# Kernel tuning notes

Measured on AMD Instinct MI355X. Metric: run time of the kernel, lower is better.

## Reference

```python
import jax, jax.numpy as jnp
import numpy as np

V, D, NL, S, B = 32000, 1024, 2, 2048, 1
EXPAND, N, K = 2, 16, 4
DI = EXPAND * D
EPS = 1e-5


def setup_inputs() -> dict:
    key = jax.random.key(0)
    ks = jax.random.split(key, 10)
    std = 0.02
    inp = {
        "input_ids": jax.random.randint(ks[0], (B, S), 0, V),
        "embedding": jax.random.normal(ks[1], (V, D), jnp.float32) * std,
        "in_proj_w": jax.random.normal(ks[2], (NL, 2 * DI, D), jnp.float32) * std,
        "conv_w": jax.random.normal(ks[3], (NL, DI, 1, K), jnp.float32) * std,
        "conv_b": jnp.zeros((NL, DI), jnp.float32),
        "x_proj_w": jax.random.normal(ks[4], (NL, 2 * N, DI), jnp.float32) * std,
        "dt_proj_w": jax.random.normal(ks[5], (NL, DI, DI), jnp.float32) * std,
        "dt_proj_b": jnp.zeros((NL, DI), jnp.float32),
        "A_log": jnp.broadcast_to(jnp.log(jnp.arange(1, N + 1, dtype=jnp.float32)), (NL, DI, N)).copy(),
        "D_param": jnp.ones((NL, DI), jnp.float32),
        "out_proj_w": jax.random.normal(ks[6], (NL, D, DI), jnp.float32) * std,
        "norm_w": jnp.ones((NL, D), jnp.float32),
        "norm_f_w": jnp.ones((D,), jnp.float32),
        "lm_head_w": jax.random.normal(ks[7], (V, D), jnp.float32) * std,
    }
    return inp


def rmsnorm(x, w):
    rms = jnp.sqrt(jnp.mean(x * x, axis=-1, keepdims=True) + EPS)
    return x / rms * w


def silu(x):
    return x * jax.nn.sigmoid(x)


def ssm_layer(x, in_w, cw, cb, xp_w, dt_w, dt_b, A_log, Dp):
    b, s, _ = x.shape
    xz = jnp.einsum("bsd,ed->bse", x, in_w)  # (B,S,2*DI)
    xi, z = jnp.split(xz, 2, axis=-1)
    # depthwise causal conv1d
    xc = jnp.swapaxes(xi, 1, 2)  # (B,DI,S)
    xc = jax.lax.conv_general_dilated(
        xc, cw, window_strides=(1,), padding=[(K - 1, 0)],
        dimension_numbers=("NCH", "OIH", "NCH"), feature_group_count=DI,
    ) + cb[None, :, None]
    xi = silu(jnp.swapaxes(xc, 1, 2))  # (B,S,DI)
    bc = jnp.einsum("bsd,ed->bse", xi, xp_w)  # (B,S,2N)
    Bc, Cc = jnp.split(bc, 2, axis=-1)
    dt = jax.nn.softplus(jnp.einsum("bsd,ed->bse", xi, dt_w) + dt_b)
    A = -jnp.exp(A_log)  # (DI,N)
    dA = jnp.exp(dt[..., None] * A)                      # (B,S,DI,N)
    dBu = dt[..., None] * Bc[:, :, None, :] * xi[..., None]  # (B,S,DI,N)

    def step(h, t):
        dA_t, dBu_t, C_t, u_t = t
        h = dA_t * h + dBu_t                     # (B,DI,N)
        y = jnp.sum(h * C_t[:, None, :], axis=-1) + Dp * u_t  # (B,DI)
        return h, y

    xs = (jnp.swapaxes(dA, 0, 1), jnp.swapaxes(dBu, 0, 1),
          jnp.swapaxes(Cc, 0, 1), jnp.swapaxes(xi, 0, 1))
    h0 = jnp.zeros((b, DI, N), x.dtype)
    _, ys = jax.lax.scan(step, h0, xs)
    y = jnp.swapaxes(ys, 0, 1)  # (B,S,DI)
    y = y * silu(z)
    return y


def reference(input_ids, embedding, in_proj_w, conv_w, conv_b, x_proj_w,
              dt_proj_w, dt_proj_b, A_log, D_param, out_proj_w, norm_w,
              norm_f_w, lm_head_w):
    x = embedding[input_ids]  # (B,S,D)
    for l in range(NL):
        h = rmsnorm(x, norm_w[l])
        y = ssm_layer(h, in_proj_w[l], conv_w[l], conv_b[l], x_proj_w[l],
                      dt_proj_w[l], dt_proj_b[l], A_log[l], D_param[l])
        x = x + jnp.einsum("bse,de->bsd", y, out_proj_w[l])
    x = rmsnorm(x, norm_f_w)
    logits = jnp.einsum("bsd,vd->bsv", x, lm_head_w)
    return logits
```

## Files before the change

kernel.cpp:

```cpp
#include <hip/hip_runtime.h>
#include <hip/hip_bf16.h>
#include <stdint.h>
#include <stddef.h>

#define Vv   32000
#define Dd   1024
#define NLay 2
#define Ss   2048
#define Nn   16
#define Kc   4
#define DIc  2048
#define EPSf 1e-5f
#define LCH  32
#define NCHc (Ss / LCH)
#define CATR 2176

typedef __attribute__((ext_vector_type(8))) short bf16x8;
typedef __attribute__((ext_vector_type(4))) float f32x4;

__device__ __forceinline__ short f2bf(float f) {
  union { float f; unsigned u; } a; a.f = f;
  return (short)((a.u + 0x7FFFu + ((a.u >> 16) & 1u)) >> 16);
}
__device__ __forceinline__ float bf2f(short s) {
  union { unsigned u; float f; } a; a.u = ((unsigned)(unsigned short)s) << 16;
  return a.f;
}

struct CvtSeg { const float* s; short* d; unsigned n4; };
struct CvtBatch { CvtSeg seg[7]; unsigned tot4; };
__global__ __launch_bounds__(256) void cvt_all_k(CvtBatch b) {
  for (unsigned idx = blockIdx.x * 256 + threadIdx.x; idx < b.tot4;
       idx += gridDim.x * 256) {
    unsigned r = idx;
    int sg = 0;
    while (sg < 6 && r >= b.seg[sg].n4) { r -= b.seg[sg].n4; ++sg; }
    float4 v = ((const float4*)b.seg[sg].s)[r];
    short4 o;
    o.x = f2bf(v.x); o.y = f2bf(v.y); o.z = f2bf(v.z); o.w = f2bf(v.w);
    ((short4*)b.seg[sg].d)[r] = o;
  }
}

__global__ __launch_bounds__(256) void embed_k(const int* __restrict__ ids,
                                               const float* __restrict__ emb,
                                               float* __restrict__ x) {
  int s = blockIdx.x;
  int id = ids[s];
  const float4* src = (const float4*)(emb + (size_t)id * Dd);
  float4* dst = (float4*)(x + (size_t)s * Dd);
  dst[threadIdx.x] = src[threadIdx.x];
}

__global__ __launch_bounds__(256) void rmsnorm_k(const float* __restrict__ x,
                                                 const float* __restrict__ w,
                                                 short* __restrict__ o) {
  int s = blockIdx.x, t = threadIdx.x;
  float4 v = ((const float4*)(x + (size_t)s * Dd))[t];
  float ss = v.x * v.x + v.y * v.y + v.z * v.z + v.w * v.w;
#pragma unroll
  for (int off = 32; off; off >>= 1) ss += __shfl_down(ss, off);
  __shared__ float red[4];
  if ((t & 63) == 0) red[t >> 6] = ss;
  __syncthreads();
  ss = red[0] + red[1] + red[2] + red[3];
  float rinv = rsqrtf(ss * (1.0f / Dd) + EPSf);
  float4 wv = ((const float4*)w)[t];
  short4 ov;
  ov.x = f2bf(v.x * rinv * wv.x);
  ov.y = f2bf(v.y * rinv * wv.y);
  ov.z = f2bf(v.z * rinv * wv.z);
  ov.w = f2bf(v.w * rinv * wv.w);
  ((short4*)(o + (size_t)s * Dd))[t] = ov;
}

template <int BM, int BN, int WM, int WN, bool RESID, bool CAT>
__global__ __launch_bounds__(256) void gemm_bt(const short* __restrict__ A,
                                               const short* __restrict__ B,
                                               float* C, const float* __restrict__ resb,
                                               float* C2, int M, int N, int K, int nMt) {
  constexpr int BK = 32;
  constexpr int FM = BM / (WM * 16);
  constexpr int FN = BN / (WN * 16);
  constexpr int A_SLOTS = BM * (BK / 8);
  constexpr int B_SLOTS = BN * (BK / 8);
  __shared__ short sA[BM * BK];
  __shared__ short sB[BN * BK];
  const int t = threadIdx.x;
  const int lane = t & 63;
  const int w = t >> 6;
  const int wm = w / WN, wn = w % WN;
  const int nwg = gridDim.x;
  const int chunk = nwg >> 3;
  const int wg = (blockIdx.x & 7) * chunk + (blockIdx.x >> 3);
  const int mi = wg % nMt;
  const int ni = wg / nMt;
  const int rowBase = mi * BM;
  const int colBase = ni * BN;
  const int l4 = lane >> 4;
  const int lr = lane & 15;
  const int mrd = ((lr & 3) ^ ((lr >> 2) & 1));

  f32x4 acc[FM][FN];
#pragma unroll
  for (int i = 0; i < FM; i++)
#pragma unroll
    for (int j = 0; j < FN; j++) acc[i][j] = f32x4{0.f, 0.f, 0.f, 0.f};

  for (int k0 = 0; k0 < K; k0 += BK) {
    __syncthreads();
#pragma unroll
    for (int i = 0; i < (A_SLOTS + 255) / 256; i++) {
      int q = i * 256 + t;
      if (A_SLOTS % 256 == 0 || q < A_SLOTS) {
        int row = q >> 2, ps = q & 3;
        int ls = ps ^ ((row & 3) ^ ((row >> 2) & 1));
        const short* src = A + (size_t)(rowBase + row) * K + (k0 + ls * 8);
        __builtin_amdgcn_global_load_lds(
            (__attribute__((address_space(1))) unsigned int*)src,
            (__attribute__((address_space(3))) unsigned int*)(sA + q * 8), 16, 0, 0);
      }
    }
#pragma unroll
    for (int i = 0; i < (B_SLOTS + 255) / 256; i++) {
      int q = i * 256 + t;
      if (B_SLOTS % 256 == 0 || q < B_SLOTS) {
        int row = q >> 2, ps = q & 3;
        int ls = ps ^ ((row & 3) ^ ((row >> 2) & 1));
        const short* src = B + (size_t)(colBase + row) * K + (k0 + ls * 8);
        __builtin_amdgcn_global_load_lds(
            (__attribute__((address_space(1))) unsigned int*)src,
            (__attribute__((address_space(3))) unsigned int*)(sB + q * 8), 16, 0, 0);
      }
    }
    __syncthreads();
    bf16x8 av[FM], bv[FN];
#pragma unroll
    for (int i = 0; i < FM; i++) {
      int row = wm * FM * 16 + i * 16 + lr;
      av[i] = *(const bf16x8*)(sA + (row * 4 + (l4 ^ mrd)) * 8);
    }
#pragma unroll
    for (int j = 0; j < FN; j++) {
      int row = wn * FN * 16 + j * 16 + lr;
      bv[j] = *(const bf16x8*)(sB + (row * 4 + (l4 ^ mrd)) * 8);
    }
#pragma unroll
    for (int i = 0; i < FM; i++)
#pragma unroll
      for (int j = 0; j < FN; j++)
        acc[i][j] = __builtin_amdgcn_mfma_f32_16x16x32_bf16(av[i], bv[j], acc[i][j], 0, 0, 0);
  }
#pragma unroll
  for (int i = 0; i < FM; i++) {
#pragma unroll
    for (int j = 0; j < FN; j++) {
      int r0 = rowBase + wm * FM * 16 + i * 16 + l4 * 4;
      int c = colBase + wn * FN * 16 + j * 16 + lr;
#pragma unroll
      for (int rr = 0; rr < 4; rr++) {
        int r = r0 + rr;
        float v = acc[i][j][rr];
        if (CAT) {
          if (c < DIc) {
            float xv = v + resb[c];
            C[(size_t)r * DIc + c] = fmaxf(xv, 0.f) + log1pf(__expf(-fabsf(xv)));
          } else if (c < DIc + 2 * Nn) {
            C2[(size_t)r * (2 * Nn) + (c - DIc)] = v;
          }
        } else {
          size_t idx = (size_t)r * N + c;
          if (RESID) v += resb[idx];
          C[idx] = v;
        }
      }
    }
  }
}

__global__ __launch_bounds__(512, 2) void gemm256(const short* __restrict__ A,
                                                  const short* __restrict__ B,
                                                  float* __restrict__ C,
                                                  int M, int N, int K, int nMt) {
  __shared__ short lds[2][2][256 * 64];
  const int t = threadIdx.x;
  const int lane = t & 63;
  const int w = t >> 6;
  const int wm = w >> 2, wn = w & 3;
  const int lr = lane & 15, l4 = lane >> 4;
  const int nwg = gridDim.x;
  const int chunk = nwg >> 3;
  const int wg = (blockIdx.x & 7) * chunk + (blockIdx.x >> 3);
  const int mi = wg % nMt, ni = wg / nMt;
  const size_t rowBase = (size_t)mi * 256, colBase = (size_t)ni * 256;

  const short* aSrc[4]; const short* bSrc[4];
  int ldsOff[4];
#pragma unroll
  for (int p = 0; p < 4; ++p) {
    int q = p * 512 + t;
    int row = q >> 3, s = q & 7;
    int ks = (s ^ (row & 7)) * 8;
    aSrc[p] = A + (rowBase + row) * K + ks;
    bSrc[p] = B + (colBase + row) * K + ks;
    ldsOff[p] = q * 8;
  }
  auto stage = [&](int buf, int k0) {
#pragma unroll
    for (int p = 0; p < 4; ++p)
      __builtin_amdgcn_global_load_lds(
          (__attribute__((address_space(1))) unsigned int*)(aSrc[p] + k0),
          (__attribute__((address_space(3))) unsigned int*)(&lds[buf][0][ldsOff[p]]), 16, 0, 0);
#pragma unroll
    for (int p = 0; p < 4; ++p)
      __builtin_amdgcn_global_load_lds(
          (__attribute__((address_space(1))) unsigned int*)(bSrc[p] + k0),
          (__attribute__((address_space(3))) unsigned int*)(&lds[buf][1][ldsOff[p]]), 16, 0, 0);
  };

  f32x4 acc[8][4];
#pragma unroll
  for (int i = 0; i < 8; i++)
#pragma unroll
    for (int j = 0; j < 4; j++) acc[i][j] = f32x4{0.f, 0.f, 0.f, 0.f};

  stage(0, 0);
  const int KT = K >> 6;
  for (int kt = 0; kt < KT; ++kt) {
    const int cur = kt & 1;
    __syncthreads();
    bf16x8 a0[4][2], b0[4][2];
#pragma unroll
    for (int i = 0; i < 4; i++)
#pragma unroll
      for (int kq = 0; kq < 2; kq++) {
        int r = wm * 128 + i * 16 + lr;
        int ks = kq * 4 + l4;
        a0[i][kq] = *(const bf16x8*)&lds[cur][0][r * 64 + ((ks ^ (r & 7)) << 3)];
      }
#pragma unroll
    for (int j = 0; j < 4; j++)
#pragma unroll
      for (int kq = 0; kq < 2; kq++) {
        int r = wn * 64 + j * 16 + lr;
        int ks = kq * 4 + l4;
        b0[j][kq] = *(const bf16x8*)&lds[cur][1][r * 64 + ((ks ^ (r & 7)) << 3)];
      }
    if (kt + 1 < KT) stage(cur ^ 1, (kt + 1) << 6);
    __builtin_amdgcn_s_setprio(1);
#pragma unroll
    for (int i = 0; i < 4; i++)
#pragma unroll
      for (int j = 0; j < 4; j++)
#pragma unroll
        for (int kq = 0; kq < 2; kq++)
          acc[i][j] = __builtin_amdgcn_mfma_f32_16x16x32_bf16(a0[i][kq], b0[j][kq], acc[i][j], 0, 0, 0);
    __builtin_amdgcn_s_setprio(0);
    bf16x8 a1[4][2];
#pragma unroll
    for (int i = 0; i < 4; i++)
#pragma unroll
      for (int kq = 0; kq < 2; kq++) {
        int r = wm * 128 + 64 + i * 16 + lr;
        int ks = kq * 4 + l4;
        a1[i][kq] = *(const bf16x8*)&lds[cur][0][r * 64 + ((ks ^ (r & 7)) << 3)];
      }
    __builtin_amdgcn_s_setprio(1);
#pragma unroll
    for (int i = 0; i < 4; i++)
#pragma unroll
      for (int j = 0; j < 4; j++)
#pragma unroll
        for (int kq = 0; kq < 2; kq++)
          acc[i + 4][j] = __builtin_amdgcn_mfma_f32_16x16x32_bf16(a1[i][kq], b0[j][kq], acc[i + 4][j], 0, 0, 0);
    __builtin_amdgcn_s_setprio(0);
  }
#pragma unroll
  for (int i = 0; i < 8; i++) {
#pragma unroll
    for (int j = 0; j < 4; j++) {
      size_t r0 = rowBase + wm * 128 + i * 16 + l4 * 4;
      size_t c = colBase + wn * 64 + j * 16 + lr;
#pragma unroll
      for (int rr = 0; rr < 4; rr++)
        C[(r0 + rr) * N + c] = acc[i][j][rr];
    }
  }
}

__global__ __launch_bounds__(256) void conv_silu_k(const float* __restrict__ xz,
                                                   const float* __restrict__ cw,
                                                   const float* __restrict__ cb,
                                                   short* __restrict__ xiC) {
  int idx = blockIdx.x * 256 + threadIdx.x;
  int s = idx / DIc, c = idx - s * DIc;
  float acc = cb[c];
  float w0 = cw[c * 4 + 0], w1 = cw[c * 4 + 1], w2 = cw[c * 4 + 2], w3 = cw[c * 4 + 3];
  float x0 = (s >= 3) ? xz[(size_t)(s - 3) * (2 * DIc) + c] : 0.f;
  float x1 = (s >= 2) ? xz[(size_t)(s - 2) * (2 * DIc) + c] : 0.f;
  float x2 = (s >= 1) ? xz[(size_t)(s - 1) * (2 * DIc) + c] : 0.f;
  float x3 = xz[(size_t)s * (2 * DIc) + c];
  acc += w0 * x0 + w1 * x1 + w2 * x2 + w3 * x3;
  float sv = acc / (1.f + __expf(-acc));
  xiC[idx] = f2bf(sv);
}

__global__ __launch_bounds__(256) void scan_pass1(const float* __restrict__ dt,
                                                  const short* __restrict__ u,
                                                  const float* __restrict__ bc,
                                                  const float* __restrict__ alog,
                                                  float* __restrict__ Ap,
                                                  float* __restrict__ Hl) {
  const int j = blockIdx.x;
  const int d = blockIdx.y * 256 + threadIdx.x;
  __shared__ float sB[LCH][Nn];
  for (int q = threadIdx.x; q < LCH * Nn; q += 256) {
    int tt = q >> 4, n = q & 15;
    sB[tt][n] = bc[(size_t)(j * LCH + tt) * 32 + n];
  }
  __syncthreads();
  float Ar[Nn], h[Nn], ap[Nn];
#pragma unroll
  for (int n = 0; n < Nn; n++) {
    Ar[n] = -__expf(alog[d * Nn + n]); h[n] = 0.f; ap[n] = 1.f;
  }
  const int t0 = j * LCH;
  for (int tt = 0; tt < LCH; tt++) {
    size_t gi = (size_t)(t0 + tt) * DIc + d;
    float dtv = dt[gi];
    float uv = bf2f(u[gi]);
    float dtu = dtv * uv;
#pragma unroll
    for (int n = 0; n < Nn; n++) {
      float a = __expf(dtv * Ar[n]);
      h[n] = a * h[n] + dtu * sB[tt][n];
      ap[n] *= a;
    }
  }
  size_t base = ((size_t)j * DIc + d) * Nn;
#pragma unroll
  for (int n = 0; n < Nn; n++) { Ap[base + n] = ap[n]; Hl[base + n] = h[n]; }
}

__global__ __launch_bounds__(256) void scan_combine(const float* __restrict__ Ap,
                                                    const float* __restrict__ Hl,
                                                    float* __restrict__ Hi) {
  int idx = blockIdx.x * 256 + threadIdx.x;
  float h = 0.f;
  for (int j = 0; j < NCHc; j++) {
    size_t o = (size_t)j * DIc * Nn + idx;
    Hi[o] = h;
    h = Ap[o] * h + Hl[o];
  }
}

__global__ __launch_bounds__(256) void scan_pass2(const float* __restrict__ dt,
                                                  const short* __restrict__ u,
                                                  const float* __restrict__ bc,
                                                  const float* __restrict__ alog,
                                                  const float* __restrict__ Hinit,
                                                  const float* __restrict__ Dp,
                                                  const float* __restrict__ xz,
                                                  short* __restrict__ y) {
  const int j = blockIdx.x;
  const int d = blockIdx.y * 256 + threadIdx.x;
  __shared__ float sB[LCH][Nn], sC[LCH][Nn];
  for (int q = threadIdx.x; q < LCH * Nn; q += 256) {
    int tt = q >> 4, n = q & 15;
    size_t r = (size_t)(j * LCH + tt) * 32;
    sB[tt][n] = bc[r + n];
    sC[tt][n] = bc[r + 16 + n];
  }
  __syncthreads();
  float Ar[Nn], h[Nn];
  size_t hb = ((size_t)j * DIc + d) * Nn;
#pragma unroll
  for (int n = 0; n < Nn; n++) {
    Ar[n] = -__expf(alog[d * Nn + n]); h[n] = Hinit[hb + n];
  }
  float dp = Dp[d];
  const int t0 = j * LCH;
  for (int tt = 0; tt < LCH; tt++) {
    size_t gi = (size_t)(t0 + tt) * DIc + d;
    float dtv = dt[gi];
    float uv = bf2f(u[gi]);
    float dtu = dtv * uv;
    float yv = dp * uv;
#pragma unroll
    for (int n = 0; n < Nn; n++) {
      float a = __expf(dtv * Ar[n]);
      h[n] = a * h[n] + dtu * sB[tt][n];
      yv += h[n] * sC[tt][n];
    }
    float zv = xz[(size_t)(t0 + tt) * (2 * DIc) + DIc + d];
    float sz = zv / (1.f + __expf(-zv));
    y[gi] = f2bf(yv * sz);
  }
}

extern "C" void kernel_launch(void* const* d_in, const int* in_sizes, int n_in,
                              void* d_out, int out_size, void* d_ws, size_t ws_size,
                              hipStream_t stream) {
  (void)in_sizes; (void)n_in; (void)out_size; (void)ws_size;
  const int* ids = (const int*)d_in[0];
  const float* emb = (const float*)d_in[1];
  const float* in_proj_w = (const float*)d_in[2];
  const float* conv_w = (const float*)d_in[3];
  const float* conv_b = (const float*)d_in[4];
  const float* x_proj_w = (const float*)d_in[5];
  const float* dt_proj_w = (const float*)d_in[6];
  const float* dt_proj_b = (const float*)d_in[7];
  const float* A_log = (const float*)d_in[8];
  const float* D_param = (const float*)d_in[9];
  const float* out_proj_w = (const float*)d_in[10];
  const float* norm_w = (const float*)d_in[11];
  const float* norm_f_w = (const float*)d_in[12];
  const float* lm_head_w = (const float*)d_in[13];
  float* logits = (float*)d_out;

  char* ws = (char*)d_ws;
  size_t woff = 0;
  auto walloc = [&](size_t bytes) { void* p = ws + woff; woff += (bytes + 255) & ~(size_t)255; return p; };
  float* x     = (float*)walloc((size_t)Ss * Dd * 4);
  short* xfbf  = (short*)walloc((size_t)Ss * Dd * 2);
  short* w_lm  = (short*)walloc((size_t)Vv * Dd * 2);

  char* sc = (char*)d_out;
  size_t soff = 0;
  auto salloc = [&](size_t bytes) { void* p = sc + soff; soff += (bytes + 255) & ~(size_t)255; return p; };
  float* xz   = (float*)salloc((size_t)Ss * 2 * DIc * 4);
  float* dtb  = (float*)salloc((size_t)Ss * DIc * 4);
  float* bc   = (float*)salloc((size_t)Ss * 32 * 4);
  float* Ap   = (float*)salloc((size_t)NCHc * DIc * Nn * 4);
  float* Hl   = (float*)salloc((size_t)NCHc * DIc * Nn * 4);
  float* Hi   = (float*)salloc((size_t)NCHc * DIc * Nn * 4);
  short* hbf  = (short*)salloc((size_t)Ss * Dd * 2);
  short* xiC  = (short*)salloc((size_t)Ss * DIc * 2);
  short* ybf  = (short*)salloc((size_t)Ss * DIc * 2);
  short* w_in = (short*)salloc((size_t)NLay * 2 * DIc * Dd * 2);
  short* w_cat= (short*)salloc((size_t)NLay * CATR * DIc * 2);
  short* w_out= (short*)salloc((size_t)NLay * Dd * DIc * 2);

  CvtBatch cb2{};
  unsigned tot = 0;
  auto addseg = [&](int i, const float* s, short* d, size_t n) {
    cb2.seg[i].s = s; cb2.seg[i].d = d; cb2.seg[i].n4 = (unsigned)(n / 4);
    tot += (unsigned)(n / 4);
  };
  addseg(0, in_proj_w, w_in, (size_t)NLay * 2 * DIc * Dd);
  addseg(1, out_proj_w, w_out, (size_t)NLay * Dd * DIc);
  addseg(2, lm_head_w, w_lm, (size_t)Vv * Dd);
  addseg(3, dt_proj_w, w_cat, (size_t)DIc * DIc);
  addseg(4, x_proj_w, w_cat + (size_t)DIc * DIc, (size_t)2 * Nn * DIc);
  addseg(5, dt_proj_w + (size_t)DIc * DIc, w_cat + (size_t)CATR * DIc, (size_t)DIc * DIc);
  addseg(6, x_proj_w + (size_t)2 * Nn * DIc,
         w_cat + (size_t)CATR * DIc + (size_t)DIc * DIc, (size_t)2 * Nn * DIc);
  cb2.tot4 = tot;
  cvt_all_k<<<dim3(4096), dim3(256), 0, stream>>>(cb2);

  embed_k<<<dim3(Ss), dim3(256), 0, stream>>>(ids, emb, x);

  for (int l = 0; l < NLay; l++) {
    rmsnorm_k<<<dim3(Ss), dim3(256), 0, stream>>>(x, norm_w + (size_t)l * Dd, hbf);
    gemm_bt<128, 128, 2, 2, false, false><<<dim3(16 * 32), dim3(256), 0, stream>>>(
        hbf, w_in + (size_t)l * 2 * DIc * Dd, xz, nullptr, nullptr, Ss, 2 * DIc, Dd, 16);
    conv_silu_k<<<dim3(Ss * DIc / 256), dim3(256), 0, stream>>>(
        xz, conv_w + (size_t)l * DIc * Kc, conv_b + (size_t)l * DIc, xiC);
    gemm_bt<128, 128, 2, 2, false, true><<<dim3(16 * 17), dim3(256), 0, stream>>>(
        xiC, w_cat + (size_t)l * CATR * DIc, dtb, dt_proj_b + (size_t)l * DIc, bc,
        Ss, CATR, DIc, 16);
    scan_pass1<<<dim3(NCHc, DIc / 256), dim3(256), 0, stream>>>(
        dtb, xiC, bc, A_log + (size_t)l * DIc * Nn, Ap, Hl);
    scan_combine<<<dim3(DIc * Nn / 256), dim3(256), 0, stream>>>(Ap, Hl, Hi);
    scan_pass2<<<dim3(NCHc, DIc / 256), dim3(256), 0, stream>>>(
        dtb, xiC, bc, A_log + (size_t)l * DIc * Nn, Hi,
        D_param + (size_t)l * DIc, xz, ybf);
    gemm_bt<128, 128, 2, 2, true, false><<<dim3(16 * 8), dim3(256), 0, stream>>>(
        ybf, w_out + (size_t)l * Dd * DIc, x, x, nullptr, Ss, Dd, DIc, 16);
  }

  rmsnorm_k<<<dim3(Ss), dim3(256), 0, stream>>>(x, norm_f_w, xfbf);
  gemm256<<<dim3(8 * 125), dim3(512), 0, stream>>>(xfbf, w_lm, logits, Ss, Vv, Dd, 8);
}
```

Baseline: 735.3 us.

## Use 256x256 four-stage pipelined GEMM for all projections and vectorize conv

Removes the 128x128 gemm_bt kernel and routes the in_proj, dt/x_proj and out_proj GEMMs through a templated gemm256 with residual and softplus epilogues. gemm256 moves from a double-buffered BK=64 loop to a four-stage BK=32 pipeline, using explicit vmcnt waits and raw barriers so global-to-LDS loads overlap MFMA work. The concatenated weight row count is padded to a multiple of 256, and the depthwise conv+SiLU kernel now processes four channels per thread with float4 loads. In exchange, the smaller GEMMs launch far fewer workgroups (32 to 128), which may leave many CUs idle.

```diff
diff --git a/kernel.cpp b/kernel.cpp
--- a/kernel.cpp
+++ b/kernel.cpp
@@ -13,7 +13,7 @@
 #define EPSf 1e-5f
 #define LCH  32
 #define NCHc (Ss / LCH)
-#define CATR 2176
+#define CATR 2304
 
 typedef __attribute__((ext_vector_type(8))) short bf16x8;
 typedef __attribute__((ext_vector_type(4))) float f32x4;
@@ -74,115 +74,14 @@
   ((short4*)(o + (size_t)s * Dd))[t] = ov;
 }
 
-template <int BM, int BN, int WM, int WN, bool RESID, bool CAT>
-__global__ __launch_bounds__(256) void gemm_bt(const short* __restrict__ A,
-                                               const short* __restrict__ B,
-                                               float* C, const float* __restrict__ resb,
-                                               float* C2, int M, int N, int K, int nMt) {
-  constexpr int BK = 32;
-  constexpr int FM = BM / (WM * 16);
-  constexpr int FN = BN / (WN * 16);
-  constexpr int A_SLOTS = BM * (BK / 8);
-  constexpr int B_SLOTS = BN * (BK / 8);
-  __shared__ short sA[BM * BK];
-  __shared__ short sB[BN * BK];
-  const int t = threadIdx.x;
-  const int lane = t & 63;
-  const int w = t >> 6;
-  const int wm = w / WN, wn = w % WN;
-  const int nwg = gridDim.x;
-  const int chunk = nwg >> 3;
-  const int wg = (blockIdx.x & 7) * chunk + (blockIdx.x >> 3);
-  const int mi = wg % nMt;
-  const int ni = wg / nMt;
-  const int rowBase = mi * BM;
-  const int colBase = ni * BN;
-  const int l4 = lane >> 4;
-  const int lr = lane & 15;
-  const int mrd = ((lr & 3) ^ ((lr >> 2) & 1));
-
-  f32x4 acc[FM][FN];
-#pragma unroll
-  for (int i = 0; i < FM; i++)
-#pragma unroll
-    for (int j = 0; j < FN; j++) acc[i][j] = f32x4{0.f, 0.f, 0.f, 0.f};
-
-  for (int k0 = 0; k0 < K; k0 += BK) {
-    __syncthreads();
-#pragma unroll
-    for (int i = 0; i < (A_SLOTS + 255) / 256; i++) {
-      int q = i * 256 + t;
-      if (A_SLOTS % 256 == 0 || q < A_SLOTS) {
-        int row = q >> 2, ps = q & 3;
-        int ls = ps ^ ((row & 3) ^ ((row >> 2) & 1));
-        const short* src = A + (size_t)(rowBase + row) * K + (k0 + ls * 8);
-        __builtin_amdgcn_global_load_lds(
-            (__attribute__((address_space(1))) unsigned int*)src,
-            (__attribute__((address_space(3))) unsigned int*)(sA + q * 8), 16, 0, 0);
-      }
-    }
-#pragma unroll
-    for (int i = 0; i < (B_SLOTS + 255) / 256; i++) {
-      int q = i * 256 + t;
-      if (B_SLOTS % 256 == 0 || q < B_SLOTS) {
-        int row = q >> 2, ps = q & 3;
-        int ls = ps ^ ((row & 3) ^ ((row >> 2) & 1));
-        const short* src = B + (size_t)(colBase + row) * K + (k0 + ls * 8);
-        __builtin_amdgcn_global_load_lds(
-            (__attribute__((address_space(1))) unsigned int*)src,
-            (__attribute__((address_space(3))) unsigned int*)(sB + q * 8), 16, 0, 0);
-      }
-    }
-    __syncthreads();
-    bf16x8 av[FM], bv[FN];
-#pragma unroll
-    for (int i = 0; i < FM; i++) {
-      int row = wm * FM * 16 + i * 16 + lr;
-      av[i] = *(const bf16x8*)(sA + (row * 4 + (l4 ^ mrd)) * 8);
-    }
-#pragma unroll
-    for (int j = 0; j < FN; j++) {
-      int row = wn * FN * 16 + j * 16 + lr;
-      bv[j] = *(const bf16x8*)(sB + (row * 4 + (l4 ^ mrd)) * 8);
-    }
-#pragma unroll
-    for (int i = 0; i < FM; i++)
-#pragma unroll
-      for (int j = 0; j < FN; j++)
-        acc[i][j] = __builtin_amdgcn_mfma_f32_16x16x32_bf16(av[i], bv[j], acc[i][j], 0, 0, 0);
-  }
-#pragma unroll
-  for (int i = 0; i < FM; i++) {
-#pragma unroll
-    for (int j = 0; j < FN; j++) {
-      int r0 = rowBase + wm * FM * 16 + i * 16 + l4 * 4;
-      int c = colBase + wn * FN * 16 + j * 16 + lr;
-#pragma unroll
-      for (int rr = 0; rr < 4; rr++) {
-        int r = r0 + rr;
-        float v = acc[i][j][rr];
-        if (CAT) {
-          if (c < DIc) {
-            float xv = v + resb[c];
-            C[(size_t)r * DIc + c] = fmaxf(xv, 0.f) + log1pf(__expf(-fabsf(xv)));
-          } else if (c < DIc + 2 * Nn) {
-            C2[(size_t)r * (2 * Nn) + (c - DIc)] = v;
-          }
-        } else {
-          size_t idx = (size_t)r * N + c;
-          if (RESID) v += resb[idx];
-          C[idx] = v;
-        }
-      }
-    }
-  }
-}
-
+template <bool RESID, bool CAT>
 __global__ __launch_bounds__(512, 2) void gemm256(const short* __restrict__ A,
                                                   const short* __restrict__ B,
                                                   float* __restrict__ C,
+                                                  const float* __restrict__ resb,
+                                                  float* __restrict__ C2,
                                                   int M, int N, int K, int nMt) {
-  __shared__ short lds[2][2][256 * 64];
+  __shared__ short lds[4][2][256 * 32];
   const int t = threadIdx.x;
   const int lane = t & 63;
   const int w = t >> 6;
@@ -194,28 +93,27 @@
   const int mi = wg % nMt, ni = wg / nMt;
   const size_t rowBase = (size_t)mi * 256, colBase = (size_t)ni * 256;
 
-  const short* aSrc[4]; const short* bSrc[4];
-  int ldsOff[4];
-#pragma unroll
-  for (int p = 0; p < 4; ++p) {
+  const short* aSrc[2]; const short* bSrc[2]; int sOff[2];
+#pragma unroll
+  for (int p = 0; p < 2; ++p) {
     int q = p * 512 + t;
-    int row = q >> 3, s = q & 7;
-    int ks = (s ^ (row & 7)) * 8;
+    int row = q >> 2, s = q & 3;
+    int ks = (s ^ (row & 3)) * 8;
     aSrc[p] = A + (rowBase + row) * K + ks;
     bSrc[p] = B + (colBase + row) * K + ks;
-    ldsOff[p] = q * 8;
+    sOff[p] = q * 8;
   }
   auto stage = [&](int buf, int k0) {
 #pragma unroll
-    for (int p = 0; p < 4; ++p)
+    for (int p = 0; p < 2; ++p)
       __builtin_amdgcn_global_load_lds(
           (__attribute__((address_space(1))) unsigned int*)(aSrc[p] + k0),
-          (__attribute__((address_space(3))) unsigned int*)(&lds[buf][0][ldsOff[p]]), 16, 0, 0);
-#pragma unroll
-    for (int p = 0; p < 4; ++p)
+          (__attribute__((address_space(3))) unsigned int*)(&lds[buf][0][sOff[p]]), 16, 0, 0);
+#pragma unroll
+    for (int p = 0; p < 2; ++p)
       __builtin_amdgcn_global_load_lds(
           (__attribute__((address_space(1))) unsigned int*)(bSrc[p] + k0),
-          (__attribute__((address_space(3))) unsigned int*)(&lds[buf][1][ldsOff[p]]), 16, 0, 0);
+          (__attribute__((address_space(3))) unsigned int*)(&lds[buf][1][sOff[p]]), 16, 0, 0);
   };
 
   f32x4 acc[8][4];
@@ -224,55 +122,37 @@
 #pragma unroll
     for (int j = 0; j < 4; j++) acc[i][j] = f32x4{0.f, 0.f, 0.f, 0.f};
 
-  stage(0, 0);
-  const int KT = K >> 6;
+  const int KT = K >> 5;
+  stage(0, 0); stage(1, 32); stage(2, 64);
   for (int kt = 0; kt < KT; ++kt) {
-    const int cur = kt & 1;
-    __syncthreads();
-    bf16x8 a0[4][2], b0[4][2];
-#pragma unroll
-    for (int i = 0; i < 4; i++)
-#pragma unroll
-      for (int kq = 0; kq < 2; kq++) {
-        int r = wm * 128 + i * 16 + lr;
-        int ks = kq * 4 + l4;
-        a0[i][kq] = *(const bf16x8*)&lds[cur][0][r * 64 + ((ks ^ (r & 7)) << 3)];
-      }
-#pragma unroll
-    for (int j = 0; j < 4; j++)
-#pragma unroll
-      for (int kq = 0; kq < 2; kq++) {
-        int r = wn * 64 + j * 16 + lr;
-        int ks = kq * 4 + l4;
-        b0[j][kq] = *(const bf16x8*)&lds[cur][1][r * 64 + ((ks ^ (r & 7)) << 3)];
-      }
-    if (kt + 1 < KT) stage(cur ^ 1, (kt + 1) << 6);
+    const int rem = KT - 1 - kt;
+    __builtin_amdgcn_sched_barrier(0);
+    if (rem >= 2)      asm volatile("s_waitcnt vmcnt(8)" ::: "memory");
+    else if (rem == 1) asm volatile("s_waitcnt vmcnt(4)" ::: "memory");
+    else               asm volatile("s_waitcnt vmcnt(0)" ::: "memory");
+    __builtin_amdgcn_sched_barrier(0);
+    __builtin_amdgcn_s_barrier();
+    __builtin_amdgcn_sched_barrier(0);
+    if (kt + 3 < KT) stage((kt + 3) & 3, (kt + 3) << 5);
+    const short* la = &lds[kt & 3][0][0];
+    const short* lb = &lds[kt & 3][1][0];
+    bf16x8 av[8], bv[4];
+#pragma unroll
+    for (int i = 0; i < 8; i++) {
+      int r = wm * 128 + i * 16 + lr;
+      av[i] = *(const bf16x8*)&la[r * 32 + ((l4 ^ (r & 3)) << 3)];
+    }
+#pragma unroll
+    for (int j = 0; j < 4; j++) {
+      int r = wn * 64 + j * 16 + lr;
+      bv[j] = *(const bf16x8*)&lb[r * 32 + ((l4 ^ (r & 3)) << 3)];
+    }
     __builtin_amdgcn_s_setprio(1);
 #pragma unroll
-    for (int i = 0; i < 4; i++)
+    for (int i = 0; i < 8; i++)
 #pragma unroll
       for (int j = 0; j < 4; j++)
-#pragma unroll
-        for (int kq = 0; kq < 2; kq++)
-          acc[i][j] = __builtin_amdgcn_mfma_f32_16x16x32_bf16(a0[i][kq], b0[j][kq], acc[i][j], 0, 0, 0);
-    __builtin_amdgcn_s_setprio(0);
-    bf16x8 a1[4][2];
-#pragma unroll
-    for (int i = 0; i < 4; i++)
-#pragma unroll
-      for (int kq = 0; kq < 2; kq++) {
-        int r = wm * 128 + 64 + i * 16 + lr;
-        int ks = kq * 4 + l4;
-        a1[i][kq] = *(const bf16x8*)&lds[cur][0][r * 64 + ((ks ^ (r & 7)) << 3)];
-      }
-    __builtin_amdgcn_s_setprio(1);
-#pragma unroll
-    for (int i = 0; i < 4; i++)
-#pragma unroll
-      for (int j = 0; j < 4; j++)
-#pragma unroll
-        for (int kq = 0; kq < 2; kq++)
-          acc[i + 4][j] = __builtin_amdgcn_mfma_f32_16x16x32_bf16(a1[i][kq], b0[j][kq], acc[i + 4][j], 0, 0, 0);
+        acc[i][j] = __builtin_amdgcn_mfma_f32_16x16x32_bf16(av[i], bv[j], acc[i][j], 0, 0, 0);
     __builtin_amdgcn_s_setprio(0);
   }
 #pragma unroll
@@ -282,8 +162,22 @@
       size_t r0 = rowBase + wm * 128 + i * 16 + l4 * 4;
       size_t c = colBase + wn * 64 + j * 16 + lr;
 #pragma unroll
-      for (int rr = 0; rr < 4; rr++)
-        C[(r0 + rr) * N + c] = acc[i][j][rr];
+      for (int rr = 0; rr < 4; rr++) {
+        size_t r = r0 + rr;
+        float v = acc[i][j][rr];
+        if (CAT) {
+          if (c < DIc) {
+            float xv = v + resb[c];
+            C[r * DIc + c] = fmaxf(xv, 0.f) + log1pf(__expf(-fabsf(xv)));
+          } else if (c < DIc + 2 * Nn) {
+            C2[r * (2 * Nn) + (c - DIc)] = v;
+          }
+        } else {
+          size_t idx = r * N + c;
+          if (RESID) v += resb[idx];
+          C[idx] = v;
+        }
+      }
     }
   }
 }
@@ -293,16 +187,28 @@
                                                    const float* __restrict__ cb,
                                                    short* __restrict__ xiC) {
   int idx = blockIdx.x * 256 + threadIdx.x;
-  int s = idx / DIc, c = idx - s * DIc;
-  float acc = cb[c];
-  float w0 = cw[c * 4 + 0], w1 = cw[c * 4 + 1], w2 = cw[c * 4 + 2], w3 = cw[c * 4 + 3];
-  float x0 = (s >= 3) ? xz[(size_t)(s - 3) * (2 * DIc) + c] : 0.f;
-  float x1 = (s >= 2) ? xz[(size_t)(s - 2) * (2 * DIc) + c] : 0.f;
-  float x2 = (s >= 1) ? xz[(size_t)(s - 1) * (2 * DIc) + c] : 0.f;
-  float x3 = xz[(size_t)s * (2 * DIc) + c];
-  acc += w0 * x0 + w1 * x1 + w2 * x2 + w3 * x3;
-  float sv = acc / (1.f + __expf(-acc));
-  xiC[idx] = f2bf(sv);
+  int s = idx / (DIc / 4), c4 = idx - s * (DIc / 4);
+  const float4* xz4 = (const float4*)xz;
+  const size_t rstride = 2 * DIc / 4;
+  float4 zero = {0.f, 0.f, 0.f, 0.f};
+  float4 x0 = (s >= 3) ? xz4[(size_t)(s - 3) * rstride + c4] : zero;
+  float4 x1 = (s >= 2) ? xz4[(size_t)(s - 2) * rstride + c4] : zero;
+  float4 x2 = (s >= 1) ? xz4[(size_t)(s - 1) * rstride + c4] : zero;
+  float4 x3 = xz4[(size_t)s * rstride + c4];
+  float4 cbv = ((const float4*)cb)[c4];
+  short4 ov;
+  float xs[4][4] = {{x0.x, x1.x, x2.x, x3.x}, {x0.y, x1.y, x2.y, x3.y},
+                    {x0.z, x1.z, x2.z, x3.z}, {x0.w, x1.w, x2.w, x3.w}};
+  float cbs[4] = {cbv.x, cbv.y, cbv.z, cbv.w};
+  short os[4];
+#pragma unroll
+  for (int j = 0; j < 4; j++) {
+    float4 wv = ((const float4*)cw)[c4 * 4 + j];
+    float acc = cbs[j] + wv.x * xs[j][0] + wv.y * xs[j][1] + wv.z * xs[j][2] + wv.w * xs[j][3];
+    os[j] = f2bf(acc / (1.f + __expf(-acc)));
+  }
+  ov.x = os[0]; ov.y = os[1]; ov.z = os[2]; ov.w = os[3];
+  ((short4*)xiC)[idx] = ov;
 }
 
 __global__ __launch_bounds__(256) void scan_pass1(const float* __restrict__ dt,
@@ -462,23 +368,24 @@
 
   for (int l = 0; l < NLay; l++) {
     rmsnorm_k<<<dim3(Ss), dim3(256), 0, stream>>>(x, norm_w + (size_t)l * Dd, hbf);
-    gemm_bt<128, 128, 2, 2, false, false><<<dim3(16 * 32), dim3(256), 0, stream>>>(
-        hbf, w_in + (size_t)l * 2 * DIc * Dd, xz, nullptr, nullptr, Ss, 2 * DIc, Dd, 16);
-    conv_silu_k<<<dim3(Ss * DIc / 256), dim3(256), 0, stream>>>(
+    gemm256<false, false><<<dim3(128), dim3(512), 0, stream>>>(
+        hbf, w_in + (size_t)l * 2 * DIc * Dd, xz, nullptr, nullptr, Ss, 2 * DIc, Dd, 8);
+    conv_silu_k<<<dim3(Ss * DIc / 4 / 256), dim3(256), 0, stream>>>(
         xz, conv_w + (size_t)l * DIc * Kc, conv_b + (size_t)l * DIc, xiC);
-    gemm_bt<128, 128, 2, 2, false, true><<<dim3(16 * 17), dim3(256), 0, stream>>>(
+    gemm256<false, true><<<dim3(72), dim3(512), 0, stream>>>(
         xiC, w_cat + (size_t)l * CATR * DIc, dtb, dt_proj_b + (size_t)l * DIc, bc,
-        Ss, CATR, DIc, 16);
+        Ss, CATR, DIc, 8);
     scan_pass1<<<dim3(NCHc, DIc / 256), dim3(256), 0, stream>>>(
         dtb, xiC, bc, A_log + (size_t)l * DIc * Nn, Ap, Hl);
     scan_combine<<<dim3(DIc * Nn / 256), dim3(256), 0, stream>>>(Ap, Hl, Hi);
     scan_pass2<<<dim3(NCHc, DIc / 256), dim3(256), 0, stream>>>(
         dtb, xiC, bc, A_log + (size_t)l * DIc * Nn, Hi,
         D_param + (size_t)l * DIc, xz, ybf);
-    gemm_bt<128, 128, 2, 2, true, false><<<dim3(16 * 8), dim3(256), 0, stream>>>(
-        ybf, w_out + (size_t)l * Dd * DIc, x, x, nullptr, Ss, Dd, DIc, 16);
+    gemm256<true, false><<<dim3(32), dim3(512), 0, stream>>>(
+        ybf, w_out + (size_t)l * Dd * DIc, x, x, nullptr, Ss, Dd, DIc, 8);
   }
 
   rmsnorm_k<<<dim3(Ss), dim3(256), 0, stream>>>(x, norm_f_w, xfbf);
-  gemm256<<<dim3(8 * 125), dim3(512), 0, stream>>>(xfbf, w_lm, logits, Ss, Vv, Dd, 8);
-}
+  gemm256<false, false><<<dim3(1000), dim3(512), 0, stream>>>(
+      xfbf, w_lm, logits, nullptr, nullptr, Ss, Vv, Dd, 8);
+}
```

Result: slower. 884.8 us (+20.3%).
